# Kernel optimization log

Measured on AMD Instinct MI355X. Metric: run time of the kernel, lower is better.

The kernel has to match this reference:

```python
import jax, jax.numpy as jnp
import numpy as np

NUM_FEATURES = 256
NUM_HEADS = 8
HEAD_SIZE = NUM_FEATURES // NUM_HEADS  # 32
N_AGENTS = 8
B = 32
SEQ = 64


def setup_inputs() -> dict:
    key = jax.random.key(0)
    ks = jax.random.split(key, 6)
    s = 0.02
    x = jax.random.normal(ks[0], (N_AGENTS * B, NUM_FEATURES, SEQ), dtype=jnp.float32)
    Wq = jax.random.normal(ks[1], (NUM_HEADS, NUM_FEATURES, HEAD_SIZE), dtype=jnp.float32) * s
    Wk = jax.random.normal(ks[2], (NUM_HEADS, NUM_FEATURES, HEAD_SIZE), dtype=jnp.float32) * s
    Wv = jax.random.normal(ks[3], (NUM_HEADS, NUM_FEATURES, HEAD_SIZE), dtype=jnp.float32) * s
    Wp = jax.random.normal(ks[4], (NUM_FEATURES, NUM_FEATURES), dtype=jnp.float32) * s
    bp = jnp.zeros((NUM_FEATURES,), dtype=jnp.float32)
    return {"x": x, "Wq": Wq, "Wk": Wk, "Wv": Wv, "Wp": Wp, "bp": bp, "n_agents": N_AGENTS}


def reference(x, Wq, Wk, Wv, Wp, bp, n_agents):
    # x: (n_agents*b, f, h)
    b_total, f, h = x.shape
    b = b_total // n_agents
    # reshape + rearrange 'n b f h -> n b h f'  (t = token axis of length h)
    xs = x.reshape(n_agents, b, f, h).transpose(0, 1, 3, 2)  # (n, b, t, f)
    # All heads at once: per-head linear projections (no bias)
    q = jnp.einsum('nbtf,Hfd->Hnbtd', xs, Wq)
    k = jnp.einsum('nbtf,Hfd->Hnbtd', xs, Wk)
    v = jnp.einsum('nbtf,Hfd->Hnbtd', xs, Wv)
    # all-pairs agent attention: i = key agent, j = query agent
    scale = f ** (-0.5)  # source scales by num_features, not head_size
    scores = jnp.einsum('Hjbtd,Hibsd->Hijbts', q, k) * scale  # (H,n,n,b,t,s)
    attn = jax.nn.softmax(scores, axis=-1)
    # weighted values, then sum over key-agent axis i
    out = jnp.einsum('Hijbts,Hibsd->Hjbtd', attn, v)  # (H,n,b,t,d)
    # concat heads on last dim (head 0 first), matching torch.cat
    y = jnp.moveaxis(out, 0, 3).reshape(n_agents, b, h, f)  # (n,b,t,H*d)
    # output projection (dropout is identity at eval / p=0)
    y = jnp.einsum('nbtf,gf->nbtg', y, Wp) + bp
    # rearrange 'n b h f -> n b f h' then merge agents into batch
    y = y.transpose(0, 1, 3, 2).reshape(n_agents * b, f, h)
    return y
```

## Files before the change

### kernel.cpp

```cpp
#include <hip/hip_runtime.h>

#define F   256
#define T   64
#define NH  8
#define D   32
#define NA  8
#define NBB 32

typedef unsigned short ushortT;
typedef unsigned int   uintT;

typedef short bf16x8 __attribute__((ext_vector_type(8)));
typedef float f32x4  __attribute__((ext_vector_type(4)));

__device__ __forceinline__ float bf2f(ushortT u) {
    union { uintT i; float f; } c; c.i = ((uintT)u) << 16; return c.f;
}
__device__ __forceinline__ ushortT f2bf(float f) {
    union { float f; uintT u; } c; c.f = f;
    uintT u = c.u;
    uintT r = u + 0x7fffu + ((u >> 16) & 1u);
    return (ushortT)(r >> 16);
}

__device__ __forceinline__ uintT cvt_pk_bf16(float lo, float hi) {
    uintT r;
    asm("v_cvt_pk_bf16_f32 %0, %1, %2" : "=v"(r) : "v"(lo), "v"(hi));
    return r;
}
__device__ __forceinline__ void packc1(const f32x4 v, uintT& u0, uintT& u1) {
    u0 = cvt_pk_bf16(v[0], v[1]);
    u1 = cvt_pk_bf16(v[2], v[3]);
}
__device__ __forceinline__ void packcs(const f32x4 v, float s, uintT& u0, uintT& u1) {
    u0 = cvt_pk_bf16(v[0] * s, v[1] * s);
    u1 = cvt_pk_bf16(v[2] * s, v[3] * s);
}

__device__ __forceinline__ float fexp2(float x) {
#if __has_builtin(__builtin_amdgcn_exp2f)
    return __builtin_amdgcn_exp2f(x);
#else
    float r; asm("v_exp_f32 %0, %1" : "=v"(r) : "v"(x)); return r;
#endif
}
__device__ __forceinline__ float frcp(float x) {
#if __has_builtin(__builtin_amdgcn_rcpf)
    return __builtin_amdgcn_rcpf(x);
#else
    float r; asm("v_rcp_f32 %0, %1" : "=v"(r) : "v"(x)); return r;
#endif
}

__device__ __forceinline__ int detect_isbf16(const void* xraw) {
    const uintT* w = (const uintT*)xraw;
    int bad = 0;
    for (int k = 0; k < 128; ++k) {
        uintT v = w[k];
        uintT e0 = (v >> 7)  & 0xffu;
        uintT e1 = (v >> 23) & 0xffu;
        bad += (e0 > 131u) + (e1 > 131u);
    }
    return bad == 0 ? 1 : 0;
}

__device__ __forceinline__ ushortT cvt_elem(const void* p, size_t i, bool isbf) {
    return isbf ? ((const ushortT*)p)[i] : f2bf(((const float*)p)[i]);
}

__device__ __forceinline__ bf16x8 build_frag(uintT u0a, uintT u1a, uintT u0b, uintT u1b,
                                             int sl0, int sl1, bool hi) {
    union { uintT u[4]; bf16x8 v; } r;
    uintT x0a = (uintT)__shfl((int)u0a, sl0), x0b = (uintT)__shfl((int)u0b, sl0);
    uintT x1a = (uintT)__shfl((int)u1a, sl0), x1b = (uintT)__shfl((int)u1b, sl0);
    uintT x2a = (uintT)__shfl((int)u0a, sl1), x2b = (uintT)__shfl((int)u0b, sl1);
    uintT x3a = (uintT)__shfl((int)u1a, sl1), x3b = (uintT)__shfl((int)u1b, sl1);
    r.u[0] = hi ? x0b : x0a;
    r.u[1] = hi ? x1b : x1a;
    r.u[2] = hi ? x2b : x2a;
    r.u[3] = hi ? x3b : x3a;
    return r.v;
}

__device__ __forceinline__ int xposU(int t, int f) {
    return t * 256 + ((((f >> 3) ^ (t & 31)) * 8) | (f & 7));
}
#define FRAGPOS(t_, ks_, quad_) \
    ((t_) * 256 + ((((4 * (ks_) + (quad_)) ^ ((t_) & 31)) * 8)))


__global__ __launch_bounds__(256) void wprep_kernel(const void* __restrict__ Wq,
                                                    const void* __restrict__ Wk,
                                                    const void* __restrict__ Wv,
                                                    const void* __restrict__ Wp,
                                                    const void* __restrict__ x,
                                                    ushortT* __restrict__ Wt) {
    __shared__ int sflag;
    if (threadIdx.x == 0) sflag = detect_isbf16(x);
    __syncthreads();
    bool isbf = sflag != 0;

    int base = (blockIdx.x * 256 + threadIdx.x) * 8;
    int cp = base >> 8, f0 = base & 255;

    ushortT tmp[8];
    if (cp < 768) {
        int qkv = cp >> 8, c = cp & 255, hh = c >> 5, d = c & 31;
        const void* W = (qkv == 0) ? Wq : (qkv == 1) ? Wk : Wv;
        #pragma unroll
        for (int jj = 0; jj < 8; ++jj)
            tmp[jj] = cvt_elem(W, (size_t)(hh * F + f0 + jj) * D + d, isbf);
    } else {
        int g = cp - 768;
        #pragma unroll
        for (int jj = 0; jj < 8; ++jj)
            tmp[jj] = cvt_elem(Wp, (size_t)g * F + f0 + jj, isbf);
    }
    *(uint4*)&Wt[base] = *(const uint4*)tmp;
}

template <int NT>
__device__ __forceinline__ void stage_xT(const void* x, int nb, ushortT* xs,
                                         bool isbf, int tid) {
    int t = tid & 63;
    int g0 = tid >> 6;
    const int GP = NT / 64;
    #pragma unroll
    for (int it = 0; it < 64 / GP; ++it) {
        int g = g0 + it * GP;
        float v0, v1, v2, v3;
        if (isbf) {
            const ushortT* xp = (const ushortT*)x + (size_t)nb * (F * T) + (size_t)g * 4 * T + t;
            v0 = bf2f(xp[0]); v1 = bf2f(xp[T]); v2 = bf2f(xp[2 * T]); v3 = bf2f(xp[3 * T]);
        } else {
            const float* xp = (const float*)x + (size_t)nb * (F * T) + (size_t)g * 4 * T + t;
            v0 = xp[0]; v1 = xp[T]; v2 = xp[2 * T]; v3 = xp[3 * T];
        }
        uintT lo  = cvt_pk_bf16(v0, v1);
        uintT hi2 = cvt_pk_bf16(v2, v3);
        *(uint2*)&xs[xposU(t & 31, g * 4) + (t >> 5) * 8192] = make_uint2(lo, hi2);
    }
}

__global__ __launch_bounds__(512) void qkv_kernel(const void* __restrict__ x,
                                                  const ushortT* __restrict__ Wt,
                                                  ushortT* __restrict__ Kws,
                                                  ushortT* __restrict__ Vws) {
    int nb = blockIdx.x;
    __shared__ __align__(16) ushortT xs[T * F];
    __shared__ int sflag;
    int tid = threadIdx.x;
    if (tid == 0) sflag = detect_isbf16(x);
    __syncthreads();
    bool isbf = sflag != 0;
    stage_xT<512>(x, nb, xs, isbf, tid);
    __syncthreads();

    int w = tid >> 6, lane = tid & 63, l15 = lane & 15, quad = lane >> 4;
    int half = w >> 2;
    int rowbase = 256 + 64 * w;

    f32x4 acc[4][4];
    #pragma unroll
    for (int a = 0; a < 4; ++a)
        #pragma unroll
        for (int c = 0; c < 4; ++c) acc[a][c] = (f32x4){0.f, 0.f, 0.f, 0.f};

    #pragma unroll
    for (int ks = 0; ks < 8; ++ks) {
        bf16x8 Bfr[4];
        #pragma unroll
        for (int nt = 0; nt < 4; ++nt) {
            int t = 16 * nt + l15;
            Bfr[nt] = *(const bf16x8*)&xs[FRAGPOS(t & 31, ks, quad) + (t >> 5) * 8192];
        }
        #pragma unroll
        for (int mt = 0; mt < 4; ++mt) {
            bf16x8 Afr = *(const bf16x8*)(Wt +
                (size_t)(rowbase + 16 * mt + l15) * 256 + ks * 32 + quad * 8);
            #pragma unroll
            for (int nt = 0; nt < 4; ++nt)
                acc[mt][nt] = __builtin_amdgcn_mfma_f32_16x16x32_bf16(Afr, Bfr[nt],
                                                                      acc[mt][nt], 0, 0, 0);
        }
    }

    #pragma unroll
    for (int mt = 0; mt < 4; ++mt) {
        int rel = 64 * (w & 3) + 16 * mt + 4 * quad;
        int hh = rel >> 5, db = rel & 31;
        #pragma unroll
        for (int nt = 0; nt < 4; ++nt) {
            int t = 16 * nt + l15;
            f32x4 v = acc[mt][nt];
            if (half == 0) {
                ushortT* dst = Kws + ((size_t)(nb * NH + hh) * T + t) * D + db;
                uintT lo  = cvt_pk_bf16(v[0], v[1]);
                uintT hi2 = cvt_pk_bf16(v[2], v[3]);
                *(uint2*)dst = make_uint2(lo, hi2);
            } else {
                uintT p0 = cvt_pk_bf16(v[0], v[1]);
                uintT p1 = cvt_pk_bf16(v[2], v[3]);
                size_t vb = (size_t)(nb * NH + hh) * D + db;
                Vws[(vb + 0) * T + t] = (ushortT)p0;
                Vws[(vb + 1) * T + t] = (ushortT)(p0 >> 16);
                Vws[(vb + 2) * T + t] = (ushortT)p1;
                Vws[(vb + 3) * T + t] = (ushortT)(p1 >> 16);
            }
        }
    }
}

__global__ __launch_bounds__(512, 2) void attn_kernel(const void* __restrict__ x,
                                                      const ushortT* __restrict__ Wt,
                                                      const ushortT* __restrict__ Kws,
                                                      const ushortT* __restrict__ Vws,
                                                      const void* __restrict__ bp,
                                                      void* __restrict__ outp) {
    __shared__ __align__(16) ushortT xs[32 * F];
    __shared__ float bpf[F];
    __shared__ int sflag;

    int tid = threadIdx.x;
    int b = blockIdx.x, j = blockIdx.y, tb = blockIdx.z;
    int nbj = j * NBB + b;

    if (tid == 0) sflag = detect_isbf16(x);
    __syncthreads();
    bool isbf = sflag != 0;

    {
        int t = tid & 31, fg = tid >> 5;
        int ta = tb * 32 + t;
        #pragma unroll
        for (int it = 0; it < 4; ++it) {
            int f0 = (fg + 16 * it) * 4;
            float v0, v1, v2, v3;
            if (isbf) {
                const ushortT* xp = (const ushortT*)x + (size_t)nbj * (F * T) +
                                    (size_t)f0 * T + ta;
                v0 = bf2f(xp[0]); v1 = bf2f(xp[T]); v2 = bf2f(xp[2 * T]); v3 = bf2f(xp[3 * T]);
            } else {
                const float* xp = (const float*)x + (size_t)nbj * (F * T) +
                                  (size_t)f0 * T + ta;
                v0 = xp[0]; v1 = xp[T]; v2 = xp[2 * T]; v3 = xp[3 * T];
            }
            uintT lo  = cvt_pk_bf16(v0, v1);
            uintT hi2 = cvt_pk_bf16(v2, v3);
            *(uint2*)&xs[xposU(t, f0)] = make_uint2(lo, hi2);
        }
    }
    if (tid < 256)
        bpf[tid] = isbf ? bf2f(((const ushortT*)bp)[tid]) : ((const float*)bp)[tid];
    __syncthreads();

    int h = tid >> 6, lane = tid & 63, l15 = lane & 15, quad = lane >> 4;
    bool hi = quad >= 2;
    int sl0 = l15 + 32 * (quad & 1), sl1 = sl0 + 16;

    const float QS = 0.0625f * 1.44269504089f;
    bf16x8 qf[2];
    {
        f32x4 qacc[2][2];
        #pragma unroll
        for (int mt = 0; mt < 2; ++mt)
            #pragma unroll
            for (int nt = 0; nt < 2; ++nt) qacc[mt][nt] = (f32x4){0.f, 0.f, 0.f, 0.f};
        #pragma unroll
        for (int ks = 0; ks < 8; ++ks) {
            bf16x8 xf[2];
            #pragma unroll
            for (int nt = 0; nt < 2; ++nt)
                xf[nt] = *(const bf16x8*)&xs[FRAGPOS(16 * nt + l15, ks, quad)];
            #pragma unroll
            for (int mt = 0; mt < 2; ++mt) {
                bf16x8 Aw = *(const bf16x8*)(Wt +
                    (size_t)(32 * h + 16 * mt + l15) * 256 + ks * 32 + quad * 8);
                #pragma unroll
                for (int nt = 0; nt < 2; ++nt)
                    qacc[mt][nt] = __builtin_amdgcn_mfma_f32_16x16x32_bf16(
                        Aw, xf[nt], qacc[mt][nt], 0, 0, 0);
            }
        }
        #pragma unroll
        for (int tt = 0; tt < 2; ++tt) {
            uintT a0, a1, b0, b1;
            packcs(qacc[0][tt], QS, a0, a1);
            packcs(qacc[1][tt], QS, b0, b1);
            qf[tt] = build_frag(a0, a1, b0, b1, sl0, sl1, hi);
        }
    }

    f32x4 oacc[2][2];
    #pragma unroll
    for (int mt = 0; mt < 2; ++mt)
        #pragma unroll
        for (int tt = 0; tt < 2; ++tt) oacc[mt][tt] = (f32x4){0.f, 0.f, 0.f, 0.f};

    for (int i = 0; i < NA; ++i) {
        int nbi = i * NBB + b;
        const ushortT* Kb = Kws + (size_t)(nbi * NH + h) * T * D;
        const ushortT* Vb = Vws + (size_t)(nbi * NH + h) * D * T;

        float psum[2] = {0.f, 0.f};
        f32x4 pv[2][2];
        #pragma unroll
        for (int mt = 0; mt < 2; ++mt)
            #pragma unroll
            for (int tt = 0; tt < 2; ++tt) pv[mt][tt] = (f32x4){0.f, 0.f, 0.f, 0.f};

        #pragma unroll
        for (int kx = 0; kx < 2; ++kx) {
            bf16x8 kfr[2];
            kfr[0] = *(const bf16x8*)(Kb + (16 * (2 * kx + 0) + l15) * D + quad * 8);
            kfr[1] = *(const bf16x8*)(Kb + (16 * (2 * kx + 1) + l15) * D + quad * 8);
            bf16x8 vf0 = *(const bf16x8*)(Vb + l15 * T + kx * 32 + quad * 8);
            bf16x8 vf1 = *(const bf16x8*)(Vb + (16 + l15) * T + kx * 32 + quad * 8);

            uintT pu0[2][2], pu1[2][2];
            #pragma unroll
            for (int sp = 0; sp < 2; ++sp) {
                #pragma unroll
                for (int tt = 0; tt < 2; ++tt) {
                    f32x4 s4 = __builtin_amdgcn_mfma_f32_16x16x32_bf16(
                        kfr[sp], qf[tt], (f32x4){0.f, 0.f, 0.f, 0.f}, 0, 0, 0);
                    float e0 = fexp2(s4[0]);
                    float e1 = fexp2(s4[1]);
                    float e2 = fexp2(s4[2]);
                    float e3 = fexp2(s4[3]);
                    psum[tt] += (e0 + e1) + (e2 + e3);
                    pu0[sp][tt] = cvt_pk_bf16(e0, e1);
                    pu1[sp][tt] = cvt_pk_bf16(e2, e3);
                }
            }
            #pragma unroll
            for (int tt = 0; tt < 2; ++tt) {
                bf16x8 pf = build_frag(pu0[0][tt], pu1[0][tt], pu0[1][tt], pu1[1][tt],
                                       sl0, sl1, hi);
                pv[0][tt] = __builtin_amdgcn_mfma_f32_16x16x32_bf16(
                    vf0, pf, pv[0][tt], 0, 0, 0);
                pv[1][tt] = __builtin_amdgcn_mfma_f32_16x16x32_bf16(
                    vf1, pf, pv[1][tt], 0, 0, 0);
            }
        }

        #pragma unroll
        for (int tt = 0; tt < 2; ++tt) {
            float s = psum[tt];
            s += __shfl_xor(s, 16);
            s += __shfl_xor(s, 32);
            float inv = frcp(s);
            #pragma unroll
            for (int mt = 0; mt < 2; ++mt)
                #pragma unroll
                for (int r = 0; r < 4; ++r)
                    oacc[mt][tt][r] = fmaf(inv, pv[mt][tt][r], oacc[mt][tt][r]);
        }
    }

    __syncthreads();
    #pragma unroll
    for (int mt = 0; mt < 2; ++mt)
        #pragma unroll
        for (int tt = 0; tt < 2; ++tt) {
            int t = 16 * tt + l15;
            int cb = 32 * h + 16 * mt + 4 * quad;
            uintT u0, u1;
            packc1(oacc[mt][tt], u0, u1);
            *(uint2*)&xs[xposU(t, cb)] = make_uint2(u0, u1);
        }
    __syncthreads();

    f32x4 cacc[2][2];
    #pragma unroll
    for (int a = 0; a < 2; ++a)
        #pragma unroll
        for (int c = 0; c < 2; ++c) cacc[a][c] = (f32x4){0.f, 0.f, 0.f, 0.f};

    #pragma unroll
    for (int ks = 0; ks < 8; ++ks) {
        bf16x8 yb[2];
        #pragma unroll
        for (int nt = 0; nt < 2; ++nt)
            yb[nt] = *(const bf16x8*)&xs[FRAGPOS(16 * nt + l15, ks, quad)];
        #pragma unroll
        for (int m2 = 0; m2 < 2; ++m2) {
            int g = 16 * (2 * h + m2) + l15;
            bf16x8 wf = *(const bf16x8*)(Wt + (size_t)(768 + g) * 256 + ks * 32 + quad * 8);
            #pragma unroll
            for (int nt = 0; nt < 2; ++nt)
                cacc[m2][nt] = __builtin_amdgcn_mfma_f32_16x16x32_bf16(
                    wf, yb[nt], cacc[m2][nt], 0, 0, 0);
        }
    }

    #pragma unroll
    for (int m2 = 0; m2 < 2; ++m2)
        #pragma unroll
        for (int nt = 0; nt < 2; ++nt) {
            int t = tb * 32 + 16 * nt + l15;
            #pragma unroll
            for (int r = 0; r < 4; ++r) {
                int g = 16 * (2 * h + m2) + 4 * quad + r;
                float val = cacc[m2][nt][r] + bpf[g];
                if (isbf)
                    ((ushortT*)outp)[(size_t)nbj * F * T + g * T + t] = f2bf(val);
                else
                    ((float*)outp)[(size_t)nbj * F * T + g * T + t] = val;
            }
        }
}

__device__ __forceinline__ float tof(ushortT u) { return bf2f(u); }
__device__ __forceinline__ float tof(float f)   { return f; }

__device__ __forceinline__ void stage_x(const void* x, size_t nb, ushortT* sX,
                                        bool isbf, int tid) {
    if (isbf) {
        const int4* xg = (const int4*)((const ushortT*)x + nb * (F * T));
        int4* xl = (int4*)sX;
        for (int kk = tid; kk < F * T / 8; kk += 512) xl[kk] = xg[kk];
    } else {
        const float4* xg = (const float4*)((const float*)x + nb * (F * T));
        for (int kk = tid; kk < F * T / 4; kk += 512) {
            float4 v = xg[kk];
            int o = kk * 4;
            sX[o + 0] = f2bf(v.x); sX[o + 1] = f2bf(v.y);
            sX[o + 2] = f2bf(v.z); sX[o + 3] = f2bf(v.w);
        }
    }
}

template <typename WT>
__device__ __forceinline__ void q_proj(const WT* __restrict__ W, const ushortT* sX,
                                       ushortT* dst, int c, int t0) {
    float acc[32];
    #pragma unroll
    for (int m = 0; m < 32; ++m) acc[m] = 0.f;
    for (int f = 0; f < F; ++f) {
        float w = tof(W[f * D]);
        const ushortT* xr = &sX[f * T + t0];
        #pragma unroll
        for (int m = 0; m < 32; ++m) acc[m] = fmaf(bf2f(xr[m]), w, acc[m]);
    }
    #pragma unroll
    for (int m = 0; m < 32; ++m) dst[(t0 + m) * F + c] = f2bf(acc[m]);
}

template <typename WT>
__device__ __forceinline__ void kv_proj(const WT* __restrict__ WK, const WT* __restrict__ WV,
                                        const ushortT* sX, ushortT* sK, ushortT* sV,
                                        int c, int t0) {
    float ak[32], av[32];
    #pragma unroll
    for (int m = 0; m < 32; ++m) { ak[m] = 0.f; av[m] = 0.f; }
    for (int f = 0; f < F; ++f) {
        float wk = tof(WK[f * D]);
        float wv = tof(WV[f * D]);
        const ushortT* xr = &sX[f * T + t0];
        #pragma unroll
        for (int m = 0; m < 32; ++m) {
            float xv = bf2f(xr[m]);
            ak[m] = fmaf(xv, wk, ak[m]);
            av[m] = fmaf(xv, wv, av[m]);
        }
    }
    #pragma unroll
    for (int m = 0; m < 32; ++m) {
        sK[(t0 + m) * F + c] = f2bf(ak[m]);
        sV[(t0 + m) * F + c] = f2bf(av[m]);
    }
}

__global__ __launch_bounds__(512) void fused_kernel(const void* __restrict__ x,
                                                    const void* __restrict__ Wq,
                                                    const void* __restrict__ Wk,
                                                    const void* __restrict__ Wv,
                                                    const void* __restrict__ Wp,
                                                    const void* __restrict__ bp,
                                                    void* __restrict__ outp) {
    __shared__ __align__(16) char smem[98304];
    __shared__ int sflag;
    ushortT* sX = (ushortT*)smem;
    ushortT* sK = (ushortT*)(smem + 32768);
    ushortT* sV = (ushortT*)(smem + 65536);
    float*   sO = (float*)smem;

    int tid = threadIdx.x;
    int b = blockIdx.x, j = blockIdx.y;
    size_t nbj = (size_t)j * NBB + b;

    if (tid == 0) sflag = detect_isbf16(x);
    __syncthreads();
    bool isbf = sflag != 0;

    stage_x(x, nbj, sX, isbf, tid);
    __syncthreads();

    int c = tid & 255, t0 = (tid >> 8) * 32;
    int hc = c >> 5, dc = c & 31;
    if (isbf) q_proj((const ushortT*)Wq + (size_t)hc * F * D + dc, sX, sK, c, t0);
    else      q_proj((const float*)Wq   + (size_t)hc * F * D + dc, sX, sK, c, t0);
    __syncthreads();

    int h = tid >> 6, t = tid & 63;
    float q[32], o[32];
    #pragma unroll
    for (int dd = 0; dd < 32; ++dd) { q[dd] = bf2f(sK[t * F + h * D + dd]); o[dd] = 0.f; }

    for (int i = 0; i < NA; ++i) {
        __syncthreads();
        stage_x(x, (size_t)(i * NBB + b), sX, isbf, tid);
        __syncthreads();
        if (isbf) kv_proj((const ushortT*)Wk + (size_t)hc * F * D + dc,
                          (const ushortT*)Wv + (size_t)hc * F * D + dc, sX, sK, sV, c, t0);
        else      kv_proj((const float*)Wk   + (size_t)hc * F * D + dc,
                          (const float*)Wv   + (size_t)hc * F * D + dc, sX, sK, sV, c, t0);
        __syncthreads();
        float l = 0.f;
        float oi[32];
        #pragma unroll
        for (int dd = 0; dd < 32; ++dd) oi[dd] = 0.f;
        for (int s = 0; s < T; ++s) {
            const ushortT* kr = &sK[s * F + h * D];
            float dot = 0.f;
            #pragma unroll
            for (int dd = 0; dd < 32; ++dd) dot = fmaf(q[dd], bf2f(kr[dd]), dot);
            float e = __expf(dot * 0.0625f);
            l += e;
            const ushortT* vr = &sV[s * F + h * D];
            #pragma unroll
            for (int dd = 0; dd < 32; ++dd) oi[dd] = fmaf(e, bf2f(vr[dd]), oi[dd]);
        }
        float inv = 1.0f / l;
        #pragma unroll
        for (int dd = 0; dd < 32; ++dd) o[dd] = fmaf(inv, oi[dd], o[dd]);
    }
    __syncthreads();

    #pragma unroll
    for (int dd = 0; dd < 32; ++dd) sO[(h * D + dd) * T + t] = o[dd];
    __syncthreads();

    {
        int g = tid >> 1, te0 = (tid & 1) * 32;
        float acc[32];
        #pragma unroll
        for (int m = 0; m < 32; ++m) acc[m] = 0.f;
        if (isbf) {
            const ushortT* Wrow = (const ushortT*)Wp + (size_t)g * F;
            for (int cc = 0; cc < F; ++cc) {
                float w = bf2f(Wrow[cc]);
                const float* yr = &sO[cc * T + te0];
                #pragma unroll
                for (int m = 0; m < 32; ++m) acc[m] = fmaf(yr[m], w, acc[m]);
            }
        } else {
            const float* Wrow = (const float*)Wp + (size_t)g * F;
            for (int cc = 0; cc < F; ++cc) {
                float w = Wrow[cc];
                const float* yr = &sO[cc * T + te0];
                #pragma unroll
                for (int m = 0; m < 32; ++m) acc[m] = fmaf(yr[m], w, acc[m]);
            }
        }
        float bias = isbf ? bf2f(((const ushortT*)bp)[g]) : ((const float*)bp)[g];
        if (isbf) {
            ushortT* ob = (ushortT*)outp + nbj * F * T + g * T + te0;
            #pragma unroll
            for (int m = 0; m < 32; ++m) ob[m] = f2bf(acc[m] + bias);
        } else {
            float* ob = (float*)outp + nbj * F * T + g * T + te0;
            #pragma unroll
            for (int m = 0; m < 32; ++m) ob[m] = acc[m] + bias;
        }
    }
}

extern "C" void kernel_launch(void* const* d_in, const int* in_sizes, int n_in,
                              void* d_out, int out_size, void* d_ws, size_t ws_size,
                              hipStream_t stream) {
    const void* x  = d_in[0];
    const void* Wq = d_in[1];
    const void* Wk = d_in[2];
    const void* Wv = d_in[3];
    const void* Wp = d_in[4];
    const void* bp = d_in[5];

    const size_t needA = 17301504;

    if (ws_size >= needA) {
        char* ws = (char*)d_ws;
        ushortT* Wt  = (ushortT*)(ws + 0);
        ushortT* Kws = (ushortT*)(ws + 524288);
        ushortT* Vws = (ushortT*)(ws + 8912896);

        wprep_kernel<<<dim3(128),      dim3(256), 0, stream>>>(Wq, Wk, Wv, Wp, x, Wt);
        qkv_kernel  <<<dim3(256),      dim3(512), 0, stream>>>(x, Wt, Kws, Vws);
        attn_kernel <<<dim3(32, 8, 2), dim3(512), 0, stream>>>(x, Wt, Kws, Vws, bp, d_out);
    } else {
        fused_kernel<<<dim3(32, 8), dim3(512), 0, stream>>>(x, Wq, Wk, Wv, Wp, bp, d_out);
    }
}
```

Baseline: 146.7 us.

## Precompute scaled Q in the QKV kernel and load it in attention

Adds a 768-thread QKV kernel that also computes Q, pre-scaled by the softmax and log2 factor, and writes it to a new workspace region. A new attention kernel then loads Q fragments directly instead of recomputing the Q projection from staged x. It also drops the x staging from the attention kernel. This removes Q work that was done redundantly per (j, time-block) launch and moves it into the earlier pass. The cost is an extra 8 MB of workspace writes and reads, and the new path runs only when the workspace is large enough.

```diff
diff --git a/kernel.cpp b/kernel.cpp
--- a/kernel.cpp
+++ b/kernel.cpp
@@ -6,6 +6,8 @@
 #define D   32
 #define NA  8
 #define NBB 32
+
+#define QSCALE (0.0625f * 1.44269504089f)
 
 typedef unsigned short ushortT;
 typedef unsigned int   uintT;
@@ -140,6 +142,232 @@
         uintT hi2 = cvt_pk_bf16(v2, v3);
         *(uint2*)&xs[xposU(t & 31, g * 4) + (t >> 5) * 8192] = make_uint2(lo, hi2);
     }
+}
+
+__global__ __launch_bounds__(768) void qkvq_kernel(const void* __restrict__ x,
+                                                   const ushortT* __restrict__ Wt,
+                                                   ushortT* __restrict__ Kws,
+                                                   ushortT* __restrict__ Vws,
+                                                   ushortT* __restrict__ Qws) {
+    int nb = blockIdx.x;
+    __shared__ __align__(16) ushortT xs[T * F];
+    __shared__ int sflag;
+    int tid = threadIdx.x;
+    if (tid == 0) sflag = detect_isbf16(x);
+    __syncthreads();
+    bool isbf = sflag != 0;
+    if (tid < 512) stage_xT<512>(x, nb, xs, isbf, tid);
+    __syncthreads();
+
+    int w = tid >> 6, lane = tid & 63, l15 = lane & 15, quad = lane >> 4;
+    int cls = w >> 2;
+    int rowbase = (cls == 2) ? 64 * (w - 8) : 256 + 64 * w;
+
+    f32x4 acc[4][4];
+    #pragma unroll
+    for (int a = 0; a < 4; ++a)
+        #pragma unroll
+        for (int c = 0; c < 4; ++c) acc[a][c] = (f32x4){0.f, 0.f, 0.f, 0.f};
+
+    #pragma unroll
+    for (int ks = 0; ks < 8; ++ks) {
+        bf16x8 Bfr[4];
+        #pragma unroll
+        for (int nt = 0; nt < 4; ++nt) {
+            int t = 16 * nt + l15;
+            Bfr[nt] = *(const bf16x8*)&xs[FRAGPOS(t & 31, ks, quad) + (t >> 5) * 8192];
+        }
+        #pragma unroll
+        for (int mt = 0; mt < 4; ++mt) {
+            bf16x8 Afr = *(const bf16x8*)(Wt +
+                (size_t)(rowbase + 16 * mt + l15) * 256 + ks * 32 + quad * 8);
+            #pragma unroll
+            for (int nt = 0; nt < 4; ++nt)
+                acc[mt][nt] = __builtin_amdgcn_mfma_f32_16x16x32_bf16(Afr, Bfr[nt],
+                                                                      acc[mt][nt], 0, 0, 0);
+        }
+    }
+
+    #pragma unroll
+    for (int mt = 0; mt < 4; ++mt) {
+        int rel = 64 * (w & 3) + 16 * mt + 4 * quad;
+        int hh = rel >> 5, db = rel & 31;
+        #pragma unroll
+        for (int nt = 0; nt < 4; ++nt) {
+            int t = 16 * nt + l15;
+            f32x4 v = acc[mt][nt];
+            if (cls == 0) {
+                ushortT* dst = Kws + ((size_t)(nb * NH + hh) * T + t) * D + db;
+                uintT lo  = cvt_pk_bf16(v[0], v[1]);
+                uintT hi2 = cvt_pk_bf16(v[2], v[3]);
+                *(uint2*)dst = make_uint2(lo, hi2);
+            } else if (cls == 1) {
+                uintT p0 = cvt_pk_bf16(v[0], v[1]);
+                uintT p1 = cvt_pk_bf16(v[2], v[3]);
+                size_t vb = (size_t)(nb * NH + hh) * D + db;
+                Vws[(vb + 0) * T + t] = (ushortT)p0;
+                Vws[(vb + 1) * T + t] = (ushortT)(p0 >> 16);
+                Vws[(vb + 2) * T + t] = (ushortT)p1;
+                Vws[(vb + 3) * T + t] = (ushortT)(p1 >> 16);
+            } else {
+                ushortT* dst = Qws + ((size_t)(nb * NH + hh) * T + t) * D + db;
+                uintT lo  = cvt_pk_bf16(v[0] * QSCALE, v[1] * QSCALE);
+                uintT hi2 = cvt_pk_bf16(v[2] * QSCALE, v[3] * QSCALE);
+                *(uint2*)dst = make_uint2(lo, hi2);
+            }
+        }
+    }
+}
+
+__global__ __launch_bounds__(512, 2) void attnq_kernel(const void* __restrict__ x,
+                                                       const ushortT* __restrict__ Wt,
+                                                       const ushortT* __restrict__ Kws,
+                                                       const ushortT* __restrict__ Vws,
+                                                       const ushortT* __restrict__ Qws,
+                                                       const void* __restrict__ bp,
+                                                       void* __restrict__ outp) {
+    __shared__ __align__(16) ushortT xs[32 * F];
+    __shared__ float bpf[F];
+    __shared__ int sflag;
+
+    int tid = threadIdx.x;
+    int b = blockIdx.x, j = blockIdx.y, tb = blockIdx.z;
+    int nbj = j * NBB + b;
+
+    if (tid == 0) sflag = detect_isbf16(x);
+    if (tid < 256)
+        bpf[tid] = 0.f;
+    __syncthreads();
+    bool isbf = sflag != 0;
+    if (tid < 256)
+        bpf[tid] = isbf ? bf2f(((const ushortT*)bp)[tid]) : ((const float*)bp)[tid];
+
+    int h = tid >> 6, lane = tid & 63, l15 = lane & 15, quad = lane >> 4;
+    bool hi = quad >= 2;
+    int sl0 = l15 + 32 * (quad & 1), sl1 = sl0 + 16;
+
+    const ushortT* Qb = Qws + ((size_t)nbj * NH + h) * T * D;
+    bf16x8 qf[2];
+    qf[0] = *(const bf16x8*)(Qb + (size_t)(tb * 32 + l15) * D + quad * 8);
+    qf[1] = *(const bf16x8*)(Qb + (size_t)(tb * 32 + 16 + l15) * D + quad * 8);
+
+    f32x4 oacc[2][2];
+    #pragma unroll
+    for (int mt = 0; mt < 2; ++mt)
+        #pragma unroll
+        for (int tt = 0; tt < 2; ++tt) oacc[mt][tt] = (f32x4){0.f, 0.f, 0.f, 0.f};
+
+    for (int i = 0; i < NA; ++i) {
+        int nbi = i * NBB + b;
+        const ushortT* Kb = Kws + (size_t)(nbi * NH + h) * T * D;
+        const ushortT* Vb = Vws + (size_t)(nbi * NH + h) * D * T;
+
+        float psum[2] = {0.f, 0.f};
+        f32x4 pv[2][2];
+        #pragma unroll
+        for (int mt = 0; mt < 2; ++mt)
+            #pragma unroll
+            for (int tt = 0; tt < 2; ++tt) pv[mt][tt] = (f32x4){0.f, 0.f, 0.f, 0.f};
+
+        #pragma unroll
+        for (int kx = 0; kx < 2; ++kx) {
+            bf16x8 kfr[2];
+            kfr[0] = *(const bf16x8*)(Kb + (16 * (2 * kx + 0) + l15) * D + quad * 8);
+            kfr[1] = *(const bf16x8*)(Kb + (16 * (2 * kx + 1) + l15) * D + quad * 8);
+            bf16x8 vf0 = *(const bf16x8*)(Vb + l15 * T + kx * 32 + quad * 8);
+            bf16x8 vf1 = *(const bf16x8*)(Vb + (16 + l15) * T + kx * 32 + quad * 8);
+
+            uintT pu0[2][2], pu1[2][2];
+            #pragma unroll
+            for (int sp = 0; sp < 2; ++sp) {
+                #pragma unroll
+                for (int tt = 0; tt < 2; ++tt) {
+                    f32x4 s4 = __builtin_amdgcn_mfma_f32_16x16x32_bf16(
+                        kfr[sp], qf[tt], (f32x4){0.f, 0.f, 0.f, 0.f}, 0, 0, 0);
+                    float e0 = fexp2(s4[0]);
+                    float e1 = fexp2(s4[1]);
+                    float e2 = fexp2(s4[2]);
+                    float e3 = fexp2(s4[3]);
+                    psum[tt] += (e0 + e1) + (e2 + e3);
+                    pu0[sp][tt] = cvt_pk_bf16(e0, e1);
+                    pu1[sp][tt] = cvt_pk_bf16(e2, e3);
+                }
+            }
+            #pragma unroll
+            for (int tt = 0; tt < 2; ++tt) {
+                bf16x8 pf = build_frag(pu0[0][tt], pu1[0][tt], pu0[1][tt], pu1[1][tt],
+                                       sl0, sl1, hi);
+                pv[0][tt] = __builtin_amdgcn_mfma_f32_16x16x32_bf16(
+                    vf0, pf, pv[0][tt], 0, 0, 0);
+                pv[1][tt] = __builtin_amdgcn_mfma_f32_16x16x32_bf16(
+                    vf1, pf, pv[1][tt], 0, 0, 0);
+            }
+        }
+
+        #pragma unroll
+        for (int tt = 0; tt < 2; ++tt) {
+            float s = psum[tt];
+            s += __shfl_xor(s, 16);
+            s += __shfl_xor(s, 32);
+            float inv = frcp(s);
+            #pragma unroll
+            for (int mt = 0; mt < 2; ++mt)
+                #pragma unroll
+                for (int r = 0; r < 4; ++r)
+                    oacc[mt][tt][r] = fmaf(inv, pv[mt][tt][r], oacc[mt][tt][r]);
+        }
+    }
+
+    #pragma unroll
+    for (int mt = 0; mt < 2; ++mt)
+        #pragma unroll
+        for (int tt = 0; tt < 2; ++tt) {
+            int t = 16 * tt + l15;
+            int cb = 32 * h + 16 * mt + 4 * quad;
+            uintT u0, u1;
+            packc1(oacc[mt][tt], u0, u1);
+            *(uint2*)&xs[xposU(t, cb)] = make_uint2(u0, u1);
+        }
+    __syncthreads();
+
+    f32x4 cacc[2][2];
+    #pragma unroll
+    for (int a = 0; a < 2; ++a)
+        #pragma unroll
+        for (int c = 0; c < 2; ++c) cacc[a][c] = (f32x4){0.f, 0.f, 0.f, 0.f};
+
+    #pragma unroll
+    for (int ks = 0; ks < 8; ++ks) {
+        bf16x8 yb[2];
+        #pragma unroll
+        for (int nt = 0; nt < 2; ++nt)
+            yb[nt] = *(const bf16x8*)&xs[FRAGPOS(16 * nt + l15, ks, quad)];
+        #pragma unroll
+        for (int m2 = 0; m2 < 2; ++m2) {
+            int g = 16 * (2 * h + m2) + l15;
+            bf16x8 wf = *(const bf16x8*)(Wt + (size_t)(768 + g) * 256 + ks * 32 + quad * 8);
+            #pragma unroll
+            for (int nt = 0; nt < 2; ++nt)
+                cacc[m2][nt] = __builtin_amdgcn_mfma_f32_16x16x32_bf16(
+                    wf, yb[nt], cacc[m2][nt], 0, 0, 0);
+        }
+    }
+
+    #pragma unroll
+    for (int m2 = 0; m2 < 2; ++m2)
+        #pragma unroll
+        for (int nt = 0; nt < 2; ++nt) {
+            int t = tb * 32 + 16 * nt + l15;
+            #pragma unroll
+            for (int r = 0; r < 4; ++r) {
+                int g = 16 * (2 * h + m2) + 4 * quad + r;
+                float val = cacc[m2][nt][r] + bpf[g];
+                if (isbf)
+                    ((ushortT*)outp)[(size_t)nbj * F * T + g * T + t] = f2bf(val);
+                else
+                    ((float*)outp)[(size_t)nbj * F * T + g * T + t] = val;
+            }
+        }
 }
 
 __global__ __launch_bounds__(512) void qkv_kernel(const void* __restrict__ x,
@@ -258,7 +486,7 @@
     bool hi = quad >= 2;
     int sl0 = l15 + 32 * (quad & 1), sl1 = sl0 + 16;
 
-    const float QS = 0.0625f * 1.44269504089f;
+    const float QS = QSCALE;
     bf16x8 qf[2];
     {
         f32x4 qacc[2][2];
@@ -588,8 +816,20 @@
     const void* bp = d_in[5];
 
     const size_t needA = 17301504;
-
-    if (ws_size >= needA) {
+    const size_t needB = needA + 8388608;
+
+    if (ws_size >= needB) {
+        char* ws = (char*)d_ws;
+        ushortT* Wt  = (ushortT*)(ws + 0);
+        ushortT* Kws = (ushortT*)(ws + 524288);
+        ushortT* Vws = (ushortT*)(ws + 8912896);
+        ushortT* Qws = (ushortT*)(ws + 17301504);
+
+        wprep_kernel<<<dim3(128),      dim3(256), 0, stream>>>(Wq, Wk, Wv, Wp, x, Wt);
+        qkvq_kernel <<<dim3(256),      dim3(768), 0, stream>>>(x, Wt, Kws, Vws, Qws);
+        attnq_kernel<<<dim3(32, 8, 2), dim3(512), 0, stream>>>(x, Wt, Kws, Vws, Qws,
+                                                               bp, d_out);
+    } else if (ws_size >= needA) {
         char* ws = (char*)d_ws;
         ushortT* Wt  = (ushortT*)(ws + 0);
         ushortT* Kws = (ushortT*)(ws + 524288);
```

After: 146.2 us (median of 2 runs). No clear change (-0.3%).
